# Optimization experiments

Hardware: AMD Instinct MI355X
Metric: run time of the kernel (lower is better)

Reference implementation:

```python
import jax, jax.numpy as jnp
import numpy as np

B, A, C = 16, 16384, 81
TOP_K = 50
CONF_THRESH = 0.5
IOU_THRESH = 0.5
VAR0, VAR1 = 0.1, 0.2          # cfg['variance']
IMG_HW = 1.0                   # cfg['min_dim']/img_size = 320/320
MIN_SIZE = 0.0
NEG = -jnp.inf


def setup_inputs() -> dict:
    key = jax.random.key(0)
    k1, k2, k3 = jax.random.split(key, 3)
    conf_preds = jax.random.uniform(k1, (B, A, C), dtype=jnp.float32)
    loc_delta = jax.random.normal(k2, (B, A, 4), dtype=jnp.float32)
    anchors = jax.random.uniform(k3, (A, 4), dtype=jnp.float32)  # cxcywh priors in [0,1)
    return {"conf_preds": conf_preds, "loc_delta": loc_delta, "anchors": anchors}


def _decode_clip(loc, anchors):
    # SSD decode: cxcy = prior_cxcy + loc_xy*v0*prior_wh ; wh = prior_wh*exp(loc_wh*v1)
    cxcy = anchors[..., :2] + loc[..., :2] * VAR0 * anchors[..., 2:]
    wh = anchors[..., 2:] * jnp.exp(loc[..., 2:] * VAR1)
    x1y1 = cxcy - wh * 0.5
    x2y2 = x1y1 + wh
    boxes = jnp.concatenate([x1y1, x2y2], axis=-1)  # [..., 4] xyxy
    return jnp.clip(boxes, 0.0, IMG_HW)            # clip_boxes_to_image((1,1))


def _nms_single(boxes, s):
    # boxes: [A,4] xyxy, s: [A] scores with invalid entries already at -inf.
    # Greedy NMS, fixed TOP_K iterations (torchvision semantics: suppress iou > thresh).
    areas = (boxes[:, 2] - boxes[:, 0]) * (boxes[:, 3] - boxes[:, 1])

    def step(s, _):
        i = jnp.argmax(s)
        take = s[i] > NEG
        b = boxes[i]
        xx1 = jnp.maximum(b[0], boxes[:, 0])
        yy1 = jnp.maximum(b[1], boxes[:, 1])
        xx2 = jnp.minimum(b[2], boxes[:, 2])
        yy2 = jnp.minimum(b[3], boxes[:, 3])
        inter = jnp.maximum(xx2 - xx1, 0.0) * jnp.maximum(yy2 - yy1, 0.0)
        iou = inter / (areas[i] + areas - inter)
        s = jnp.where(take & (iou > IOU_THRESH), NEG, s)
        s = s.at[i].set(NEG)  # guarantee progress
        return s, (i, take)

    _, (idx, take) = jax.lax.scan(step, s, None, length=TOP_K)
    return idx, take  # [TOP_K] int, [TOP_K] bool


def reference(conf_preds, loc_delta, anchors):
    boxes = _decode_clip(loc_delta, anchors)                # [B,A,4]
    conf = jnp.transpose(conf_preds, (0, 2, 1))             # [B,C,A]
    # remove_small_boxes(min_size=0) as a mask (all-true here, kept for fidelity)
    w = boxes[..., 2] - boxes[..., 0]
    h = boxes[..., 3] - boxes[..., 1]
    valid = (w >= MIN_SIZE) & (h >= MIN_SIZE)               # [B,A]
    masked = jnp.where((conf > CONF_THRESH) & valid[:, None, :], conf, NEG)  # [B,C,A]

    sg = jax.lax.stop_gradient
    nms_c = jax.vmap(_nms_single, in_axes=(None, 0))        # over classes
    nms_bc = jax.vmap(nms_c, in_axes=(0, 0))                # over batch
    idx, take = nms_bc(sg(boxes), sg(masked))               # [B,C,K]

    scores_sel = jnp.take_along_axis(conf, idx, axis=2)     # [B,C,K]
    b_idx = jnp.arange(boxes.shape[0])[:, None, None]
    boxes_sel = boxes[b_idx, idx]                           # [B,C,K,4]
    preds = jnp.concatenate([
        jnp.where(take, scores_sel, 0.0)[..., None],
        jnp.where(take[..., None], boxes_sel, 0.0),
    ], axis=-1)                                             # [B,C,K,5]
    return preds
```

## Files before the change

kernel.cpp:

```cpp
#include <hip/hip_runtime.h>
#include <math.h>

#define NB 16
#define NA 16384
#define NC 81
#define TOPK 50
#define NBK 255
#define TRC 8960
#define NEGF (-__builtin_inff())
#define SUPC 0.5000000298023223876953125

typedef unsigned long long ull;

#define WS_CONFT_OFF  ((size_t)4194304)
#define WS_FULL  (WS_CONFT_OFF + (size_t)NB * NC * NA)

__device__ __forceinline__ bool iou_gt_half(float inter, float den) {
    return fmaf(den, -0.5f, inter) > den * 0x1p-25f;
}

__device__ __forceinline__ unsigned enc8(float v) {
    unsigned e = 0xFFu;
    if (v > 0.5f) {
        unsigned d = 255u - ((__float_as_uint(v) >> 15) & 0xFFu);
        e = (d > 254u) ? 254u : d;
    }
    return e;
}

__device__ __forceinline__ void decode_body(int i, const float* __restrict__ loc,
                                            const float* __restrict__ anc,
                                            float* __restrict__ boxes) {
#pragma clang fp contract(off)
    int a = i & (NA - 1);
    float4 an = ((const float4*)anc)[a];
    float4 ld = ((const float4*)loc)[i];
    float cx = an.x + (ld.x * 0.1f) * an.z;
    float cy = an.y + (ld.y * 0.1f) * an.w;
    float w = an.z * (float)exp((double)(ld.z * 0.2f));
    float h = an.w * (float)exp((double)(ld.w * 0.2f));
    float x1 = cx - w * 0.5f;
    float y1 = cy - h * 0.5f;
    float x2 = x1 + w;
    float y2 = y1 + h;
    x1 = fminf(fmaxf(x1, 0.f), 1.f);
    y1 = fminf(fmaxf(y1, 0.f), 1.f);
    x2 = fminf(fmaxf(x2, 0.f), 1.f);
    y2 = fminf(fmaxf(y2, 0.f), 1.f);
    ((float4*)boxes)[i] = make_float4(x1, y1, x2, y2);
}

__global__ __launch_bounds__(256) void decode_k(const float* __restrict__ loc,
                                                const float* __restrict__ anc,
                                                float* __restrict__ boxes) {
    int i = blockIdx.x * 256 + threadIdx.x;
    if (i < NB * NA) decode_body(i, loc, anc, boxes);
}

#define TSLAB 256
__global__ __launch_bounds__(256) void prep_k(const float* __restrict__ conf,
                                              const float* __restrict__ loc,
                                              const float* __restrict__ anc,
                                              float* __restrict__ boxes,
                                              unsigned char* __restrict__ confT) {
    __shared__ unsigned char code[TSLAB * NC];
    const int t = threadIdx.x;
    if (blockIdx.z == 1) {
        int i = (blockIdx.x + 64 * blockIdx.y) * 256 + t;
        if (i < NB * NA) decode_body(i, loc, anc, boxes);
        return;
    }
    const int b = blockIdx.y, slab = blockIdx.x;
    const float4* src = (const float4*)(conf + ((size_t)b * NA + (size_t)slab * TSLAB) * NC);
    for (int i = t; i < (TSLAB * NC) / 4; i += 256) {
        float4 v = src[i];
        unsigned wrd = enc8(v.x) | (enc8(v.y) << 8) | (enc8(v.z) << 16) | (enc8(v.w) << 24);
        *(unsigned*)&code[4 * i] = wrd;
    }
    __syncthreads();
    const int lane = t & 63, wv = t >> 6;
    for (int c = wv; c < NC; c += 4) {
        unsigned v = 0u;
#pragma unroll
        for (int j = 0; j < 4; ++j)
            v |= (unsigned)code[(4 * lane + j) * NC + c] << (8 * j);
        *(unsigned*)(confT + ((size_t)b * NC + c) * NA + (size_t)slab * TSLAB + 4 * lane) = v;
    }
}

__global__ __launch_bounds__(256, 6) void nmsB6_k(const unsigned char* __restrict__ confT,
                                                  const float* __restrict__ conf,
                                                  const float* __restrict__ boxes,
                                                  float* __restrict__ out) {
#pragma clang fp contract(off)
    const int blk = blockIdx.x;
    const int b = blk / NC, c = blk - b * NC;
    const int t = threadIdx.x;
    const int lane = t & 63, wv = t >> 6;

    __shared__ unsigned short s_ix[TRC];
    __shared__ unsigned s_off[NBK + 1];
    __shared__ unsigned s_aux[NBK];
    __shared__ float4 s_abox[TOPK];
    __shared__ float s_aarea[TOPK];
    __shared__ float4 s_cbox[256];
    __shared__ unsigned long long s_kill[4];
    __shared__ int s_ctrl[16];

    const uint4* row16 = (const uint4*)(confT + ((size_t)b * NC + c) * NA);
    const float* cp = conf + ((size_t)b * NA) * NC + c;
    const float4* bb = (const float4*)boxes + (size_t)b * NA;
    float* orow = out + ((size_t)b * NC + c) * (TOPK * 5);

    if (t < NBK) s_aux[t] = 0u;
    if (t == 0) { s_ctrl[0] = 0; s_ctrl[8] = 0; s_ctrl[12] = 0; }
    __syncthreads();
#pragma unroll
    for (int r = 0; r < 4; ++r) {
        uint4 q = row16[t + 256 * r];
        unsigned wrds[4] = {q.x, q.y, q.z, q.w};
#pragma unroll
        for (int m = 0; m < 4; ++m)
#pragma unroll
            for (int k = 0; k < 4; ++k) {
                unsigned bk = (wrds[m] >> (8 * k)) & 0xFFu;
                if (bk != 0xFFu) atomicAdd(&s_aux[bk], 1u);
            }
    }
    __syncthreads();
    if (t < NBK) atomicMax(&s_ctrl[8], (int)s_aux[t]);
    if (t == 0) s_off[0] = 0u;
    if (t < NBK) s_off[t + 1] = s_aux[t];
    __syncthreads();
    for (int d = 1; d < 256; d <<= 1) {
        unsigned v0 = 0u;
        if (t < NBK) v0 = (1 + t - d >= 1) ? s_off[1 + t - d] : 0u;
        __syncthreads();
        if (t < NBK) s_off[1 + t] += v0;
        __syncthreads();
    }

    if (s_ctrl[8] <= TRC) {
        while (true) {
            if (t == 0) {
                int lo = s_ctrl[12];
                int hi = lo;
                while (hi < NBK && s_off[hi + 1] - s_off[lo] <= (unsigned)TRC) hi++;
                s_ctrl[13] = hi;
            }
            __syncthreads();
            const int trLo = s_ctrl[12], trHi = s_ctrl[13];
            const unsigned tbase = s_off[trLo], tend = s_off[trHi];
            if (tbase == tend) break;
            for (int i = trLo + t; i < trHi; i += 256) s_aux[i] = s_off[i] - tbase;
            __syncthreads();
#pragma unroll
            for (int r = 0; r < 4; ++r) {
                uint4 q = row16[t + 256 * r];
                unsigned wrds[4] = {q.x, q.y, q.z, q.w};
                int base_a = 16 * (t + 256 * r);
#pragma unroll
                for (int m = 0; m < 4; ++m)
#pragma unroll
                    for (int k = 0; k < 4; ++k) {
                        int bk = (int)((wrds[m] >> (8 * k)) & 0xFFu);
                        if (bk >= trLo && bk < trHi)
                            s_ix[atomicAdd(&s_aux[bk], 1u)] =
                                (unsigned short)(base_a + 4 * m + k);
                    }
            }
            if (t == 0) s_ctrl[7] = trLo;
            __syncthreads();

            while (true) {
                if (t == 0) {
                    int bp = s_ctrl[7];
                    int mode;
                    if (bp >= trHi || s_off[bp] >= tend) {
                        mode = 2;
                    } else {
                        unsigned pos = s_off[bp] - tbase;
                        int bpl = bp;
                        unsigned q = pos;
                        for (int w = 0; w < 4; ++w) {
                            s_ctrl[2 + w] = (int)q;
                            while (bpl < trHi && (s_off[bpl + 1] - tbase - q) <= 64u) bpl++;
                            q = (bpl < trHi) ? s_off[bpl] - tbase : tend - tbase;
                        }
                        s_ctrl[6] = (int)q;
                        s_ctrl[7] = bpl;
                        mode = 0;
                        if (q == pos) {
                            mode = 1;
                            s_ctrl[9] = (int)pos;
                            s_ctrl[10] = (int)(s_off[bp + 1] - tbase);
                            s_ctrl[7] = bp + 1;
                        }
                    }
                    s_ctrl[11] = mode;
                }
                __syncthreads();
                const int mode = s_ctrl[11];
                if (mode == 2) break;
                const int nacc0 = s_ctrl[0];

                if (mode == 0) {
                    const unsigned q0 = (unsigned)s_ctrl[2 + wv];
                    const unsigned q1 = (unsigned)s_ctrl[3 + wv];
                    const int mw = (int)(q1 - q0);
                    const bool valid = lane < mw;
                    int ii = (int)q0 + lane; if (ii > TRC - 1) ii = TRC - 1;
                    int a = valid ? (int)s_ix[ii] : 0;
                    float4 bxv = bb[a];
                    if (!valid) bxv = make_float4(0.f, 0.f, 0.f, 0.f);
                    s_cbox[wv * 64 + lane] = bxv;
                    float mar = (bxv.z - bxv.x) * (bxv.w - bxv.y);
                    bool kill = !valid;
                    for (int j = 0; j < nacc0; ++j) {
                        float4 ab = s_abox[j];
                        float aa = s_aarea[j];
                        float xx1 = fmaxf(ab.x, bxv.x), yy1 = fmaxf(ab.y, bxv.y);
                        float xx2 = fminf(ab.z, bxv.z), yy2 = fminf(ab.w, bxv.w);
                        float iw = fmaxf(xx2 - xx1, 0.f), ih = fmaxf(yy2 - yy1, 0.f);
                        float inter = iw * ih;
                        float den = (aa + mar) - inter;
                        if (iou_gt_half(inter, den)) kill = true;
                    }
                    unsigned long long km = __ballot(kill);
                    if (lane == 0) s_kill[wv] = km;
                    __syncthreads();

                    if (wv == 0) {
                        int na = nacc0;
                        for (int cc = 0; cc < 4 && na < TOPK; ++cc) {
                            const unsigned e0 = (unsigned)s_ctrl[2 + cc];
                            const unsigned e1 = (unsigned)s_ctrl[3 + cc];
                            const int mc = (int)(e1 - e0);
                            if (mc <= 0) continue;
                            unsigned long long alive = ~s_kill[cc];
                            if (mc < 64) alive &= (1ull << mc) - 1ull;
                            int jj = (int)e0 + lane; if (jj > TRC - 1) jj = TRC - 1;
                            int aj = (lane < mc) ? (int)s_ix[jj] : 0;
                            float myscore = cp[(size_t)aj * NC];
                            float4 mybx = s_cbox[cc * 64 + lane];
                            float mar2 = (mybx.z - mybx.x) * (mybx.w - mybx.y);
                            for (int j = nacc0; j < na && alive; ++j) {
                                float4 ab = s_abox[j];
                                float aa = s_aarea[j];
                                float xx1 = fmaxf(ab.x, mybx.x), yy1 = fmaxf(ab.y, mybx.y);
                                float xx2 = fminf(ab.z, mybx.z), yy2 = fminf(ab.w, mybx.w);
                                float iw = fmaxf(xx2 - xx1, 0.f), ih = fmaxf(yy2 - yy1, 0.f);
                                float inter = iw * ih;
                                float den = (aa + mar2) - inter;
                                bool sup = iou_gt_half(inter, den);
                                alive &= ~__ballot(sup);
                            }
                            unsigned long long mykey =
                                ((unsigned long long)__float_as_uint(myscore) << 32) |
                                (unsigned)(16383 - aj);
                            while (alive && na < TOPK) {
                                unsigned long long kk = ((alive >> lane) & 1ull) ? mykey : 0ull;
                                int src = lane;
                                for (int off = 32; off; off >>= 1) {
                                    unsigned long long ok = __shfl_xor(kk, off);
                                    int osrc = __shfl_xor(src, off);
                                    if (ok > kk) { kk = ok; src = osrc; }
                                }
                                float4 wb = s_cbox[cc * 64 + src];
                                float wscore = __shfl(myscore, src);
                                float war = (wb.z - wb.x) * (wb.w - wb.y);
                                if (lane == 0) {
                                    orow[na * 5 + 0] = wscore;
                                    orow[na * 5 + 1] = wb.x; orow[na * 5 + 2] = wb.y;
                                    orow[na * 5 + 3] = wb.z; orow[na * 5 + 4] = wb.w;
                                    s_abox[na] = wb;
                                    s_aarea[na] = war;
                                }
                                na++;
                                alive &= ~(1ull << src);
                                if (alive) {
                                    float xx1 = fmaxf(wb.x, mybx.x), yy1 = fmaxf(wb.y, mybx.y);
                                    float xx2 = fminf(wb.z, mybx.z), yy2 = fminf(wb.w, mybx.w);
                                    float iw = fmaxf(xx2 - xx1, 0.f), ih = fmaxf(yy2 - yy1, 0.f);
                                    float inter = iw * ih;
                                    float den = (war + mar2) - inter;
                                    bool sup = iou_gt_half(inter, den);
                                    alive &= ~__ballot(sup);
                                }
                            }
                        }
                        if (lane == 0) s_ctrl[0] = na;
                    }
                    __syncthreads();
                } else {
                    const int e0 = s_ctrl[9], e1 = s_ctrl[10];
                    if (wv == 0) {
                        int na = s_ctrl[0];
                        while (na < TOPK) {
                            unsigned long long bk = 0ull; int bpos = 0;
                            for (int i = e0 + lane; i < e1; i += 64) {
                                int av = (int)s_ix[i];
                                if (av != 0xFFFF) {
                                    float v = cp[(size_t)av * NC];
                                    unsigned long long k =
                                        ((unsigned long long)__float_as_uint(v) << 32) |
                                        (unsigned)(16383 - av);
                                    if (k > bk) { bk = k; bpos = i; }
                                }
                            }
                            for (int off = 32; off; off >>= 1) {
                                unsigned long long ok = __shfl_xor(bk, off);
                                int op = __shfl_xor(bpos, off);
                                if (ok > bk) { bk = ok; bpos = op; }
                            }
                            if (bk == 0ull) break;
                            int a = (int)s_ix[bpos];
                            float wscore = __uint_as_float((unsigned)(bk >> 32));
                            if (lane == 0) s_ix[bpos] = 0xFFFFu;
                            float4 wb = bb[a];
                            float war = (wb.z - wb.x) * (wb.w - wb.y);
                            bool sup = false;
                            if (lane < na) {
                                float4 ab = s_abox[lane];
                                float aa = s_aarea[lane];
                                float xx1 = fmaxf(ab.x, wb.x), yy1 = fmaxf(ab.y, wb.y);
                                float xx2 = fminf(ab.z, wb.z), yy2 = fminf(ab.w, wb.w);
                                float iw = fmaxf(xx2 - xx1, 0.f), ih = fmaxf(yy2 - yy1, 0.f);
                                float inter = iw * ih;
                                float den = (aa + war) - inter;
                                sup = iou_gt_half(inter, den);
                            }
                            if (__ballot(sup) == 0ull) {
                                if (lane == 0) {
                                    orow[na * 5 + 0] = wscore;
                                    orow[na * 5 + 1] = wb.x; orow[na * 5 + 2] = wb.y;
                                    orow[na * 5 + 3] = wb.z; orow[na * 5 + 4] = wb.w;
                                    s_abox[na] = wb;
                                    s_aarea[na] = war;
                                }
                                na++;
                            }
                        }
                        if (lane == 0) s_ctrl[0] = na;
                    }
                    __syncthreads();
                }
                if (s_ctrl[0] >= TOPK) break;
            }
            if (s_ctrl[0] >= TOPK || trHi >= NBK) break;
            if (t == 0) s_ctrl[12] = trHi;
            __syncthreads();
        }
    } else {
        float hi = 1.0f, delta = 0.02f;
        while (true) {
            if (s_ctrl[0] >= TOPK || hi <= 0.5f) break;
            float lo = fmaxf(hi - delta, 0.5f);
            if (t == 0) s_ctrl[1] = 0;
            __syncthreads();
            for (int a = t; a < NA; a += 256) {
                float v = cp[(size_t)a * NC];
                if (v > lo && v <= hi) {
                    int p = atomicAdd(&s_ctrl[1], 1);
                    if (p < TRC) s_ix[p] = (unsigned short)a;
                }
            }
            __syncthreads();
            int m = s_ctrl[1];
            if (m > TRC) { delta *= 0.5f; continue; }
            if (wv == 0) {
                int na = s_ctrl[0];
                while (na < TOPK) {
                    unsigned long long bk = 0ull; int bpos = 0;
                    for (int i = lane; i < m; i += 64) {
                        int av = (int)s_ix[i];
                        if (av != 0xFFFF) {
                            float v = cp[(size_t)av * NC];
                            unsigned long long k =
                                ((unsigned long long)__float_as_uint(v) << 32) |
                                (unsigned)(16383 - av);
                            if (k > bk) { bk = k; bpos = i; }
                        }
                    }
                    for (int off = 32; off; off >>= 1) {
                        unsigned long long ok = __shfl_xor(bk, off);
                        int op = __shfl_xor(bpos, off);
                        if (ok > bk) { bk = ok; bpos = op; }
                    }
                    if (bk == 0ull) break;
                    int a = (int)s_ix[bpos];
                    float wscore = __uint_as_float((unsigned)(bk >> 32));
                    if (lane == 0) s_ix[bpos] = 0xFFFFu;
                    float4 wb = bb[a];
                    float war = (wb.z - wb.x) * (wb.w - wb.y);
                    bool sup = false;
                    if (lane < na) {
                        float4 ab = s_abox[lane];
                        float aa = s_aarea[lane];
                        float xx1 = fmaxf(ab.x, wb.x), yy1 = fmaxf(ab.y, wb.y);
                        float xx2 = fminf(ab.z, wb.z), yy2 = fminf(ab.w, wb.w);
                        float iw = fmaxf(xx2 - xx1, 0.f), ih = fmaxf(yy2 - yy1, 0.f);
                        float inter = iw * ih;
                        float den = (aa + war) - inter;
                        sup = iou_gt_half(inter, den);
                    }
                    if (__ballot(sup) == 0ull) {
                        if (lane == 0) {
                            orow[na * 5 + 0] = wscore;
                            orow[na * 5 + 1] = wb.x; orow[na * 5 + 2] = wb.y;
                            orow[na * 5 + 3] = wb.z; orow[na * 5 + 4] = wb.w;
                            s_abox[na] = wb;
                            s_aarea[na] = war;
                        }
                        na++;
                    }
                }
                if (lane == 0) s_ctrl[0] = na;
            }
            __syncthreads();
            hi = lo;
        }
    }

    __syncthreads();
    const int naF = s_ctrl[0];
    for (int z = naF * 5 + t; z < TOPK * 5; z += 256) orow[z] = 0.f;
}

#define OTHREADS 1024
#define OCAP 10240
#define OJMAX 10

__global__ __launch_bounds__(OTHREADS) void nms_old_k(const float* __restrict__ conf,
                                                      const float* __restrict__ boxes,
                                                      float* __restrict__ out) {
#pragma clang fp contract(off)
    const int blk = blockIdx.x;
    const int b = blk / NC, c = blk - b * NC;
    const int t = threadIdx.x;
    const int lane = t & 63, wid = t >> 6;
    __shared__ float s_val[OCAP];
    __shared__ unsigned short s_idx[OCAP];
    __shared__ float s_ps[2][16];
    __shared__ int s_pa[2][16];
    __shared__ int s_n;
    if (t == 0) s_n = 0;
    __syncthreads();
    const float* cp = conf + ((size_t)b * NA) * NC + c;
    float v[NA / OTHREADS];
#pragma unroll
    for (int r = 0; r < NA / OTHREADS; ++r)
        v[r] = cp[(size_t)(r * OTHREADS + t) * NC];
#pragma unroll
    for (int r = 0; r < NA / OTHREADS; ++r) {
        int a = r * OTHREADS + t;
        bool alive = v[r] > 0.5f;
        unsigned long long m = __ballot(alive);
        int cnt = __popcll(m);
        int base = 0;
        if (lane == 0 && cnt) base = atomicAdd(&s_n, cnt);
        base = __shfl(base, 0);
        if (alive) {
            int p = base + __popcll(m & ((1ull << lane) - 1));
            if (p < OCAP) { s_val[p] = v[r]; s_idx[p] = (unsigned short)a; }
        }
    }
    __syncthreads();
    int n = s_n; if (n > OCAP) n = OCAP;
    const int jn = (n + OTHREADS - 1) / OTHREADS;
    const float4* bb = (const float4*)boxes + (size_t)b * NA;
    float sc[OJMAX]; float4 bx[OJMAX]; int ia[OJMAX];
#pragma unroll
    for (int j = 0; j < OJMAX; ++j) {
        sc[j] = NEGF; ia[j] = 0x7fffffff; bx[j] = make_float4(0.f, 0.f, 0.f, 0.f);
        int p = j * OTHREADS + t;
        if (p < n) { sc[j] = s_val[p]; ia[j] = (int)s_idx[p]; bx[j] = bb[ia[j]]; }
    }
    float* orow = out + (size_t)blk * (TOPK * 5);
    int k = 0;
    for (; k < TOPK; ++k) {
        float ms = NEGF; int ma = 0x7fffffff;
#pragma unroll
        for (int j = 0; j < OJMAX; ++j) {
            if (j < jn) {
                bool better = (sc[j] > ms) || (sc[j] == ms && ia[j] < ma);
                ms = better ? sc[j] : ms;
                ma = better ? ia[j] : ma;
            }
        }
#pragma unroll
        for (int off = 32; off; off >>= 1) {
            float os = __shfl_xor(ms, off);
            int oa = __shfl_xor(ma, off);
            if (os > ms || (os == ms && oa < ma)) { ms = os; ma = oa; }
        }
        int pb = k & 1;
        if (lane == 0) { s_ps[pb][wid] = ms; s_pa[pb][wid] = ma; }
        __syncthreads();
        float wsv = NEGF; int wa = 0x7fffffff;
#pragma unroll
        for (int w = 0; w < 16; ++w) {
            float os = s_ps[pb][w]; int oa = s_pa[pb][w];
            if (os > wsv || (os == wsv && oa < wa)) { wsv = os; wa = oa; }
        }
        if (!(wsv > NEGF)) break;
        float4 wb = bb[wa];
        float warea = (wb.z - wb.x) * (wb.w - wb.y);
        if (t == 0) {
            orow[k * 5 + 0] = wsv;
            orow[k * 5 + 1] = wb.x; orow[k * 5 + 2] = wb.y;
            orow[k * 5 + 3] = wb.z; orow[k * 5 + 4] = wb.w;
        }
#pragma unroll
        for (int j = 0; j < OJMAX; ++j) {
            if (j < jn) {
                float xx1 = fmaxf(wb.x, bx[j].x);
                float yy1 = fmaxf(wb.y, bx[j].y);
                float xx2 = fminf(wb.z, bx[j].z);
                float yy2 = fminf(wb.w, bx[j].w);
                float iw = fmaxf(xx2 - xx1, 0.f);
                float ih = fmaxf(yy2 - yy1, 0.f);
                float inter = iw * ih;
                float aj = (bx[j].z - bx[j].x) * (bx[j].w - bx[j].y);
                float denom = (warea + aj) - inter;
                bool supp = ((double)inter > (double)denom * SUPC) || (ia[j] == wa);
                if (supp) sc[j] = NEGF;
            }
        }
    }
    for (int z = k * 5 + t; z < TOPK * 5; z += OTHREADS) orow[z] = 0.f;
}

extern "C" void kernel_launch(void* const* d_in, const int* in_sizes, int n_in,
                              void* d_out, int out_size, void* d_ws, size_t ws_size,
                              hipStream_t stream) {
    const float* conf = (const float*)d_in[0];
    const float* loc  = (const float*)d_in[1];
    const float* anc  = (const float*)d_in[2];
    float* boxes = (float*)d_ws;

    if (ws_size >= WS_FULL) {
        unsigned char* confT = (unsigned char*)((char*)d_ws + WS_CONFT_OFF);
        dim3 tg(NA / TSLAB, NB, 2);
        prep_k<<<tg, 256, 0, stream>>>(conf, loc, anc, boxes, confT);
        nmsB6_k<<<NB * NC, 256, 0, stream>>>(confT, conf, boxes, (float*)d_out);
    } else {
        decode_k<<<(NB * NA + 255) / 256, 256, 0, stream>>>(loc, anc, boxes);
        nms_old_k<<<NB * NC, OTHREADS, 0, stream>>>(conf, boxes, (float*)d_out);
    }
}
```

Baseline: 210.4 us.

## Keep conf codes in registers, use per-wave histograms and shuffle scan, shrink staging

The NMS kernel now loads each class row's 8-bit codes into registers once and reuses them for both the histogram and the scatter passes, instead of reading global memory twice. The histogram is split per wavefront to cut LDS atomic contention, and the barrier-heavy Hillis-Steele prefix scan is replaced by a wave shuffle scan plus a cross-wave sum. The shared staging array shrinks from 8960 to 1024 entries, which reduces LDS use and may allow more resident blocks. In exchange, more passes over the bucket tiles are needed, and the fallback path is taken whenever any bucket holds more than 1024 entries.

```diff
diff --git a/kernel.cpp b/kernel.cpp
--- a/kernel.cpp
+++ b/kernel.cpp
@@ -6,7 +6,7 @@
 #define NC 81
 #define TOPK 50
 #define NBK 255
-#define TRC 8960
+#define TRC 1024
 #define NEGF (-__builtin_inff())
 #define SUPC 0.5000000298023223876953125
 
@@ -88,7 +88,35 @@
     }
 }
 
-__global__ __launch_bounds__(256, 6) void nmsB6_k(const unsigned char* __restrict__ confT,
+#define HIST16(Q)                                                          \
+    do {                                                                   \
+        unsigned wrds_[4] = {(Q).x, (Q).y, (Q).z, (Q).w};                  \
+        _Pragma("unroll")                                                  \
+        for (int m_ = 0; m_ < 4; ++m_) {                                   \
+            _Pragma("unroll")                                              \
+            for (int k_ = 0; k_ < 4; ++k_) {                               \
+                unsigned bk_ = (wrds_[m_] >> (8 * k_)) & 0xFFu;            \
+                if (bk_ != 0xFFu) atomicAdd(&s_hist[wv][bk_], 1u);         \
+            }                                                              \
+        }                                                                  \
+    } while (0)
+
+#define SCAT16(Q, BA)                                                      \
+    do {                                                                   \
+        unsigned wrds_[4] = {(Q).x, (Q).y, (Q).z, (Q).w};                  \
+        _Pragma("unroll")                                                  \
+        for (int m_ = 0; m_ < 4; ++m_) {                                   \
+            _Pragma("unroll")                                              \
+            for (int k_ = 0; k_ < 4; ++k_) {                               \
+                int bk_ = (int)((wrds_[m_] >> (8 * k_)) & 0xFFu);          \
+                if (bk_ >= trLo && bk_ < trHi)                             \
+                    s_ix[atomicAdd(&s_cur[bk_], 1u)] =                     \
+                        (unsigned short)((BA) + 4 * m_ + k_);              \
+            }                                                              \
+        }                                                                  \
+    } while (0)
+
+__global__ __launch_bounds__(256, 6) void nmsB7_k(const unsigned char* __restrict__ confT,
                                                   const float* __restrict__ conf,
                                                   const float* __restrict__ boxes,
                                                   float* __restrict__ out) {
@@ -100,7 +128,9 @@
 
     __shared__ unsigned short s_ix[TRC];
     __shared__ unsigned s_off[NBK + 1];
-    __shared__ unsigned s_aux[NBK];
+    __shared__ unsigned s_hist[4][NBK + 2];
+    __shared__ unsigned s_cur[NBK];
+    __shared__ unsigned s_wsum[4];
     __shared__ float4 s_abox[TOPK];
     __shared__ float s_aarea[TOPK];
     __shared__ float4 s_cbox[256];
@@ -112,33 +142,37 @@
     const float4* bb = (const float4*)boxes + (size_t)b * NA;
     float* orow = out + ((size_t)b * NC + c) * (TOPK * 5);
 
-    if (t < NBK) s_aux[t] = 0u;
+    uint4 r0 = row16[t];
+    uint4 r1 = row16[t + 256];
+    uint4 r2 = row16[t + 512];
+    uint4 r3 = row16[t + 768];
+
+    for (int i = t; i < 4 * (NBK + 2); i += 256) ((unsigned*)s_hist)[i] = 0u;
     if (t == 0) { s_ctrl[0] = 0; s_ctrl[8] = 0; s_ctrl[12] = 0; }
     __syncthreads();
-#pragma unroll
-    for (int r = 0; r < 4; ++r) {
-        uint4 q = row16[t + 256 * r];
-        unsigned wrds[4] = {q.x, q.y, q.z, q.w};
-#pragma unroll
-        for (int m = 0; m < 4; ++m)
-#pragma unroll
-            for (int k = 0; k < 4; ++k) {
-                unsigned bk = (wrds[m] >> (8 * k)) & 0xFFu;
-                if (bk != 0xFFu) atomicAdd(&s_aux[bk], 1u);
-            }
-    }
-    __syncthreads();
-    if (t < NBK) atomicMax(&s_ctrl[8], (int)s_aux[t]);
+
+    HIST16(r0); HIST16(r1); HIST16(r2); HIST16(r3);
+    __syncthreads();
+
+    unsigned cnt = 0u;
+    if (t < NBK) {
+        cnt = s_hist[0][t] + s_hist[1][t] + s_hist[2][t] + s_hist[3][t];
+        atomicMax(&s_ctrl[8], (int)cnt);
+    }
+    unsigned v = cnt;
+#pragma unroll
+    for (int off = 1; off < 64; off <<= 1) {
+        unsigned o = __shfl_up(v, off);
+        if (lane >= off) v += o;
+    }
+    if (lane == 63) s_wsum[wv] = v;
+    __syncthreads();
+    unsigned basep = 0u;
+    for (int w2 = 0; w2 < wv; ++w2) basep += s_wsum[w2];
+    v += basep;
+    if (t < NBK) s_off[t + 1] = v;
     if (t == 0) s_off[0] = 0u;
-    if (t < NBK) s_off[t + 1] = s_aux[t];
-    __syncthreads();
-    for (int d = 1; d < 256; d <<= 1) {
-        unsigned v0 = 0u;
-        if (t < NBK) v0 = (1 + t - d >= 1) ? s_off[1 + t - d] : 0u;
-        __syncthreads();
-        if (t < NBK) s_off[1 + t] += v0;
-        __syncthreads();
-    }
+    __syncthreads();
 
     if (s_ctrl[8] <= TRC) {
         while (true) {
@@ -152,23 +186,12 @@
             const int trLo = s_ctrl[12], trHi = s_ctrl[13];
             const unsigned tbase = s_off[trLo], tend = s_off[trHi];
             if (tbase == tend) break;
-            for (int i = trLo + t; i < trHi; i += 256) s_aux[i] = s_off[i] - tbase;
-            __syncthreads();
-#pragma unroll
-            for (int r = 0; r < 4; ++r) {
-                uint4 q = row16[t + 256 * r];
-                unsigned wrds[4] = {q.x, q.y, q.z, q.w};
-                int base_a = 16 * (t + 256 * r);
-#pragma unroll
-                for (int m = 0; m < 4; ++m)
-#pragma unroll
-                    for (int k = 0; k < 4; ++k) {
-                        int bk = (int)((wrds[m] >> (8 * k)) & 0xFFu);
-                        if (bk >= trLo && bk < trHi)
-                            s_ix[atomicAdd(&s_aux[bk], 1u)] =
-                                (unsigned short)(base_a + 4 * m + k);
-                    }
-            }
+            for (int i = trLo + t; i < trHi; i += 256) s_cur[i] = s_off[i] - tbase;
+            __syncthreads();
+            SCAT16(r0, 16 * t);
+            SCAT16(r1, 16 * (t + 256));
+            SCAT16(r2, 16 * (t + 512));
+            SCAT16(r3, 16 * (t + 768));
             if (t == 0) s_ctrl[7] = trLo;
             __syncthreads();
 
@@ -301,9 +324,9 @@
                             for (int i = e0 + lane; i < e1; i += 64) {
                                 int av = (int)s_ix[i];
                                 if (av != 0xFFFF) {
-                                    float v = cp[(size_t)av * NC];
+                                    float vv = cp[(size_t)av * NC];
                                     unsigned long long k =
-                                        ((unsigned long long)__float_as_uint(v) << 32) |
+                                        ((unsigned long long)__float_as_uint(vv) << 32) |
                                         (unsigned)(16383 - av);
                                     if (k > bk) { bk = k; bpos = i; }
                                 }
@@ -359,8 +382,8 @@
             if (t == 0) s_ctrl[1] = 0;
             __syncthreads();
             for (int a = t; a < NA; a += 256) {
-                float v = cp[(size_t)a * NC];
-                if (v > lo && v <= hi) {
+                float vv = cp[(size_t)a * NC];
+                if (vv > lo && vv <= hi) {
                     int p = atomicAdd(&s_ctrl[1], 1);
                     if (p < TRC) s_ix[p] = (unsigned short)a;
                 }
@@ -375,9 +398,9 @@
                     for (int i = lane; i < m; i += 64) {
                         int av = (int)s_ix[i];
                         if (av != 0xFFFF) {
-                            float v = cp[(size_t)av * NC];
+                            float vv = cp[(size_t)av * NC];
                             unsigned long long k =
-                                ((unsigned long long)__float_as_uint(v) << 32) |
+                                ((unsigned long long)__float_as_uint(vv) << 32) |
                                 (unsigned)(16383 - av);
                             if (k > bk) { bk = k; bpos = i; }
                         }
@@ -543,7 +566,7 @@
         unsigned char* confT = (unsigned char*)((char*)d_ws + WS_CONFT_OFF);
         dim3 tg(NA / TSLAB, NB, 2);
         prep_k<<<tg, 256, 0, stream>>>(conf, loc, anc, boxes, confT);
-        nmsB6_k<<<NB * NC, 256, 0, stream>>>(confT, conf, boxes, (float*)d_out);
+        nmsB7_k<<<NB * NC, 256, 0, stream>>>(confT, conf, boxes, (float*)d_out);
     } else {
         decode_k<<<(NB * NA + 255) / 256, 256, 0, stream>>>(loc, anc, boxes);
         nms_old_k<<<NB * NC, OTHREADS, 0, stream>>>(conf, boxes, (float*)d_out);
```

Result: slower. 237.7 us (+13.0%).
